# Kernel optimization log

Hardware: AMD Instinct MI355X
Metric: run time of the kernel (lower is better)

Reference implementation:

```python
import jax, jax.numpy as jnp
import numpy as np

D_MODEL = 1024
N_HEAD = 16
STRIDE = 1024
SEQ = STRIDE + 1  # time_mask is (stride+1, stride+1) -> N must equal stride+1
BATCH = 4
EPS = 1e-5


def layer_norm(x, g, b):
    mu = jnp.mean(x, axis=-1, keepdims=True)
    var = jnp.var(x, axis=-1, keepdims=True)
    return (x - mu) * jax.lax.rsqrt(var + EPS) * g + b


def quick_gelu(x):
    return x * jax.nn.sigmoid(1.702 * x)


def setup_inputs() -> dict:
    key = jax.random.key(0)
    ks = jax.random.split(key, 12)
    C = D_MODEL
    s = 0.02
    return {
        "x": jax.random.normal(ks[0], (SEQ, BATCH, C), dtype=jnp.float32),
        "qkv_w": jax.random.normal(ks[1], (3 * C, C), dtype=jnp.float32) * s,
        "proj_w": jax.random.normal(ks[2], (C, C), dtype=jnp.float32) * s,
        "proj_b": jnp.zeros((C,), dtype=jnp.float32),
        "ln1_g": jnp.ones((C,), dtype=jnp.float32),
        "ln1_b": jnp.zeros((C,), dtype=jnp.float32),
        "ln2_g": jnp.ones((C,), dtype=jnp.float32),
        "ln2_b": jnp.zeros((C,), dtype=jnp.float32),
        "fc_w": jax.random.normal(ks[3], (4 * C, C), dtype=jnp.float32) * s,
        "fc_b": jnp.zeros((4 * C,), dtype=jnp.float32),
        "cproj_w": jax.random.normal(ks[4], (C, 4 * C), dtype=jnp.float32) * s,
        "cproj_b": jnp.zeros((C,), dtype=jnp.float32),
    }


def _attention(xs, qkv_w, proj_w, proj_b):
    # xs: [N, B, C] (seq-first) -> internal [B, N, C]
    xb = jnp.transpose(xs, (1, 0, 2))
    B, N, C = xb.shape
    H, Dh = N_HEAD, C // N_HEAD
    scale = Dh ** -0.5
    qkv = xb @ qkv_w.T  # [B, N, 3C], no bias (qkv_bias=False)
    qkv = qkv.reshape(B, N, 3, H, Dh).transpose(2, 0, 3, 1, 4)  # [3, B, H, N, Dh]
    q, k, v = qkv[0], qkv[1], qkv[2]
    attn = jnp.einsum("bhnd,bhmd->bhnm", q, k) * scale
    mask = jnp.tril(jnp.ones((N, N), dtype=bool))  # time_mask: causal tril
    attn = jnp.where(mask, attn, -jnp.inf)
    attn = jax.nn.softmax(attn, axis=-1)
    out = jnp.einsum("bhnm,bhmd->bhnd", attn, v)  # [B, H, N, Dh]
    out = out.transpose(0, 2, 1, 3).reshape(B, N, C)
    out = out @ proj_w.T + proj_b
    return jnp.transpose(out, (1, 0, 2)), attn  # back to [N, B, C]


def reference(x, qkv_w, proj_w, proj_b, ln1_g, ln1_b, ln2_g, ln2_b,
              fc_w, fc_b, cproj_w, cproj_b):
    y, attn = _attention(layer_norm(x, ln1_g, ln1_b), qkv_w, proj_w, proj_b)
    x = x + y
    h = layer_norm(x, ln2_g, ln2_b)
    h = quick_gelu(h @ fc_w.T + fc_b) @ cproj_w.T + cproj_b
    x = x + h
    return (x, attn)
```

## Files before the change

### kernel.cpp

```cpp
#include <hip/hip_runtime.h>


typedef unsigned short ushort_t;
typedef __bf16 bf16x8 __attribute__((ext_vector_type(8)));
typedef float f32x4 __attribute__((ext_vector_type(4)));

#define SEQ_N   1025
#define CMODEL  1024
#define NHEAD   16
#define DH      64
#define TTOK    4100
#define MP      4224
#define NPAD    1152
#define BH      64

__device__ __forceinline__ ushort_t f2bf(float f) {
  union { float f; unsigned u; } v; v.f = f;
  unsigned r = v.u + 0x7fffu + ((v.u >> 16) & 1u);
  return (ushort_t)(r >> 16);
}

__device__ __forceinline__ void gl_lds16(const void* g, void* s) {
  __builtin_amdgcn_global_load_lds(
      (const __attribute__((address_space(1))) unsigned int*)g,
      (__attribute__((address_space(3))) unsigned int*)s, 16, 0, 0);
}

__global__ __launch_bounds__(256)
void cvt4(const float* __restrict__ s0, ushort_t* __restrict__ d0,
          const float* __restrict__ s1, ushort_t* __restrict__ d1,
          const float* __restrict__ s2, ushort_t* __restrict__ d2,
          const float* __restrict__ s3, ushort_t* __restrict__ d3) {
  const int b = blockIdx.x;
  const float* s; ushort_t* d; int off;
  if (b < 3072)      { s = s0; d = d0; off = b; }
  else if (b < 4096) { s = s1; d = d1; off = b - 3072; }
  else if (b < 8192) { s = s2; d = d2; off = b - 4096; }
  else               { s = s3; d = d3; off = b - 8192; }
  const int i = (off * 256 + threadIdx.x) * 4;
  const float4 f = *(const float4*)(s + i);
  ushort4 o;
  o.x = f2bf(f.x); o.y = f2bf(f.y); o.z = f2bf(f.z); o.w = f2bf(f.w);
  *(ushort4*)(d + i) = o;
}

__global__ __launch_bounds__(256)
void ln_bf(const float* __restrict__ xin, const float* __restrict__ g,
           const float* __restrict__ bb, ushort_t* __restrict__ out,
           const float* __restrict__ rbias, float* __restrict__ resout) {
  const int t = blockIdx.x;
  const float* row = xin + (size_t)t * CMODEL;
  const int base = threadIdx.x * 4;
  const float4 v = *(const float4*)(row + base);
  float s = v.x + v.y + v.z + v.w;
  float q = v.x * v.x + v.y * v.y + v.z * v.z + v.w * v.w;
#pragma unroll
  for (int off = 32; off > 0; off >>= 1) {
    s += __shfl_down(s, off);
    q += __shfl_down(q, off);
  }
  __shared__ float sh[8];
  const int wave = threadIdx.x >> 6, lane = threadIdx.x & 63;
  if (lane == 0) { sh[wave] = s; sh[4 + wave] = q; }
  __syncthreads();
  if (threadIdx.x == 0) {
    const float ts = sh[0] + sh[1] + sh[2] + sh[3];
    const float tq = sh[4] + sh[5] + sh[6] + sh[7];
    const float mean = ts * (1.f / CMODEL);
    const float var = tq * (1.f / CMODEL) - mean * mean;
    sh[0] = mean; sh[1] = rsqrtf(var + 1e-5f);
  }
  __syncthreads();
  const float mean = sh[0], rstd = sh[1];
  const float4 gg = *(const float4*)(g + base);
  const float4 bv = *(const float4*)(bb + base);
  ushort4 o;
  o.x = f2bf((v.x - mean) * rstd * gg.x + bv.x);
  o.y = f2bf((v.y - mean) * rstd * gg.y + bv.y);
  o.z = f2bf((v.z - mean) * rstd * gg.z + bv.z);
  o.w = f2bf((v.w - mean) * rstd * gg.w + bv.w);
  *(ushort4*)(out + (size_t)t * CMODEL + base) = o;
  if (resout) {
    const float4 rb = *(const float4*)(rbias + base);
    float4 ro;
    ro.x = v.x + rb.x; ro.y = v.y + rb.y; ro.z = v.z + rb.z; ro.w = v.w + rb.w;
    *(float4*)(resout + (size_t)t * CMODEL + base) = ro;
  }
}

template <int EPI>
__global__ __launch_bounds__(256)
void gemm_bt(const ushort_t* __restrict__ A, int lda,
             const ushort_t* __restrict__ B, int ldb,
             int K,
             const float* __restrict__ bias, const float* __restrict__ res,
             float* __restrict__ outf, ushort_t* __restrict__ outb,
             ushort_t* __restrict__ oq, ushort_t* __restrict__ ok,
             ushort_t* __restrict__ ovt) {
  __shared__ __align__(16) ushort_t lsA[128 * 32];
  __shared__ __align__(16) ushort_t lsB[128 * 32];
  const int tid = threadIdx.x;
  const int wave = tid >> 6, lane = tid & 63;
  const int lr = lane & 15, quad = lane >> 4;

  const int gx = gridDim.x, gy = gridDim.y;
  const int nwg = gx * gy * gridDim.z;
  int lin = blockIdx.x + gx * (blockIdx.y + gy * blockIdx.z);
  lin = (lin & 7) * (nwg >> 3) + (lin >> 3);
  const int bx = lin % gx;
  const int byz = lin / gx;
  const int by = byz % gy;
  const int bz = byz / gy;

  const int tM = by * 128, tN = bx * 128;
  const int kbase = bz * K;
  const int waveM = (wave >> 1) * 64, waveN = (wave & 1) * 64;

  f32x4 acc[4][4];
  const f32x4 z4 = {0.f, 0.f, 0.f, 0.f};
#pragma unroll
  for (int i = 0; i < 4; ++i)
#pragma unroll
    for (int j = 0; j < 4; ++j) acc[i][j] = z4;

  for (int k0 = 0; k0 < K; k0 += 32) {
    __syncthreads();
#pragma unroll
    for (int p = 0; p < 2; ++p) {
      const int idx = p * 256 + wave * 64 + lane;
      const int row = idx >> 2, part = idx & 3;
      const int cb = (p * 256 + wave * 64) * 8;
      gl_lds16(A + (size_t)(tM + row) * lda + kbase + k0 + part * 8, lsA + cb);
      gl_lds16(B + (size_t)(tN + row) * ldb + kbase + k0 + part * 8, lsB + cb);
    }
    __syncthreads();
    bf16x8 af[4], bfr[4];
#pragma unroll
    for (int mi = 0; mi < 4; ++mi)
      af[mi] = *(const bf16x8*)(lsA + (waveM + mi * 16 + lr) * 32 + quad * 8);
#pragma unroll
    for (int ni = 0; ni < 4; ++ni)
      bfr[ni] = *(const bf16x8*)(lsB + (waveN + ni * 16 + lr) * 32 + quad * 8);
#pragma unroll
    for (int mi = 0; mi < 4; ++mi)
#pragma unroll
      for (int ni = 0; ni < 4; ++ni)
        acc[mi][ni] = __builtin_amdgcn_mfma_f32_16x16x32_bf16(af[mi], bfr[ni], acc[mi][ni], 0, 0, 0);
  }

#pragma unroll
  for (int mi = 0; mi < 4; ++mi) {
#pragma unroll
    for (int ni = 0; ni < 4; ++ni) {
#pragma unroll
      for (int r = 0; r < 4; ++r) {
        const int m = tM + waveM + mi * 16 + quad * 4 + r;
        const int n = tN + waveN + ni * 16 + lr;
        const float v = acc[mi][ni][r];
        if constexpr (EPI == 0) {
          if (m < TTOK) {
            const int b_ = m & 3, ns = m >> 2;
            const int which = n >> 10, rem = n & 1023, h = rem >> 6, d = rem & 63;
            const int bh = b_ * NHEAD + h;
            const ushort_t bv = f2bf(v);
            if (which == 0)      oq[((size_t)bh * NPAD + ns) * DH + d] = bv;
            else if (which == 1) ok[((size_t)bh * NPAD + ns) * DH + d] = bv;
            else                 ovt[((size_t)bh * DH + d) * NPAD + ns] = bv;
          }
        } else if constexpr (EPI == 3) {
          if (m < TTOK)
            outf[(size_t)m * CMODEL + n] = v + bias[n] + res[(size_t)m * CMODEL + n];
        } else if constexpr (EPI == 4) {
          if (m < TTOK) {
            const float zv = v + bias[n];
            outb[(size_t)m * 4096 + n] = f2bf(zv / (1.f + __expf(-1.702f * zv)));
          }
        } else if constexpr (EPI == 5) {
          if (m < TTOK)
            atomicAdd(outf + (size_t)m * CMODEL + n, v);
        }
      }
    }
  }
}

__global__ __launch_bounds__(256)
void attn_fused(const ushort_t* __restrict__ qb, const ushort_t* __restrict__ kb,
                const ushort_t* __restrict__ vtb, float* __restrict__ attn,
                ushort_t* __restrict__ ao) {
  __shared__ __align__(16) char smem[34816 + 17408 + 512];
  ushort_t* lsK  = (ushort_t*)smem;
  ushort_t* lsP  = (ushort_t*)smem;
  float*    lpart = (float*)smem;
  ushort_t* lsQV = (ushort_t*)(smem + 34816);
  float*    linvs = (float*)(smem + 34816 + 17408);

  int lin = blockIdx.x + 64 * blockIdx.y;
  lin = (lin & 7) * 72 + (lin >> 3);
  const int bh = lin / 9;
  const int iT = 8 - (lin % 9);
  const int tM = iT * 128;
  const int tid = threadIdx.x;
  const int wave = tid >> 6, lane = tid & 63;
  const int lr = lane & 15, quad = lane >> 4;
  const int waveM = (wave >> 1) * 64, waveN = (wave & 1) * 64;

  const ushort_t* Qg = qb + (size_t)bh * NPAD * DH;
  const ushort_t* Kg = kb + (size_t)bh * NPAD * DH;
  const ushort_t* Vg = vtb + (size_t)bh * DH * NPAD;
  float* attn_h = attn + (size_t)bh * ((size_t)SEQ_N * SEQ_N);

#pragma unroll
  for (int p = 0; p < 4; ++p) {
    const int c = p * 256 + wave * 64 + lane;
    const int ks = c >> 9, n = (c >> 2) & 127, part = c & 3;
    gl_lds16(Qg + (size_t)(tM + n) * DH + ks * 32 + part * 8,
             lsQV + (size_t)(p * 256 + wave * 64) * 8);
  }
  __syncthreads();
  bf16x8 aq[4][2];
#pragma unroll
  for (int mi = 0; mi < 4; ++mi)
#pragma unroll
    for (int ks = 0; ks < 2; ++ks)
      aq[mi][ks] = *(const bf16x8*)(lsQV + ks * 4096 + (waveM + mi * 16 + lr) * 32 + quad * 8);
  __syncthreads();

  f32x4 acc[4][4];
  const f32x4 z4 = {0.f, 0.f, 0.f, 0.f};

  float lsum[4][4];
#pragma unroll
  for (int mi = 0; mi < 4; ++mi)
#pragma unroll
    for (int r = 0; r < 4; ++r) lsum[mi][r] = 0.f;

  for (int j = 0; j <= iT; ++j) {
    __syncthreads();
#pragma unroll
    for (int p = 0; p < 4; ++p) {
      const int c = p * 256 + wave * 64 + lane;
      const int ks = c >> 9, n = (c >> 2) & 127, part = c & 3;
      gl_lds16(Kg + (size_t)(j * 128 + n) * DH + ks * 32 + part * 8,
               lsK + (size_t)(p * 256 + wave * 64) * 8);
    }
    __syncthreads();
#pragma unroll
    for (int mi = 0; mi < 4; ++mi)
#pragma unroll
      for (int ni = 0; ni < 4; ++ni) acc[mi][ni] = z4;
    __builtin_amdgcn_s_setprio(1);
#pragma unroll
    for (int ks = 0; ks < 2; ++ks) {
      bf16x8 bk[4];
#pragma unroll
      for (int ni = 0; ni < 4; ++ni)
        bk[ni] = *(const bf16x8*)(lsK + ks * 4096 + (waveN + ni * 16 + lr) * 32 + quad * 8);
#pragma unroll
      for (int mi = 0; mi < 4; ++mi)
#pragma unroll
        for (int ni = 0; ni < 4; ++ni)
          acc[mi][ni] = __builtin_amdgcn_mfma_f32_16x16x32_bf16(aq[mi][ks], bk[ni], acc[mi][ni], 0, 0, 0);
    }
    __builtin_amdgcn_s_setprio(0);
#pragma unroll
    for (int mi = 0; mi < 4; ++mi)
#pragma unroll
      for (int ni = 0; ni < 4; ++ni)
#pragma unroll
        for (int r = 0; r < 4; ++r) {
          const int row = tM + waveM + mi * 16 + quad * 4 + r;
          const int col = j * 128 + waveN + ni * 16 + lr;
          if (col <= row) lsum[mi][r] += __expf(acc[mi][ni][r] * 0.125f);
        }
  }
#pragma unroll
  for (int mi = 0; mi < 4; ++mi)
#pragma unroll
    for (int r = 0; r < 4; ++r) {
      float s = lsum[mi][r];
      s += __shfl_xor(s, 1); s += __shfl_xor(s, 2);
      s += __shfl_xor(s, 4); s += __shfl_xor(s, 8);
      lsum[mi][r] = s;
    }
  __syncthreads();
  if (lr == 0) {
    const int wx = wave & 1;
#pragma unroll
    for (int mi = 0; mi < 4; ++mi)
#pragma unroll
      for (int r = 0; r < 4; ++r)
        lpart[wx * 128 + waveM + mi * 16 + quad * 4 + r] = lsum[mi][r];
  }
  __syncthreads();
  if (tid < 128) linvs[tid] = 1.0f / (lpart[tid] + lpart[128 + tid]);
  __syncthreads();
  float linv[4][4];
#pragma unroll
  for (int mi = 0; mi < 4; ++mi)
#pragma unroll
    for (int r = 0; r < 4; ++r)
      linv[mi][r] = linvs[waveM + mi * 16 + quad * 4 + r];

  f32x4 oacc[2][4];
#pragma unroll
  for (int i = 0; i < 2; ++i)
#pragma unroll
    for (int j = 0; j < 4; ++j) oacc[i][j] = z4;
  const int prow = wave * 32;
  const int wrow = wave * 32;
  const int lcol = lane;

  for (int j = 0; j <= iT; ++j) {
    __syncthreads();
#pragma unroll
    for (int p = 0; p < 4; ++p) {
      const int c = p * 256 + wave * 64 + lane;
      const int ks = c >> 9, n = (c >> 2) & 127, part = c & 3;
      gl_lds16(Kg + (size_t)(j * 128 + n) * DH + ks * 32 + part * 8,
               lsK + (size_t)(p * 256 + wave * 64) * 8);
    }
#pragma unroll
    for (int p = 0; p < 4; ++p) {
      const int c = p * 256 + tid;
      const int n = c >> 4, klc = c & 15;
      const uint4 v = *(const uint4*)(Vg + (size_t)n * NPAD + j * 128 + klc * 8);
      *(uint4*)(lsQV + (size_t)n * 136 + klc * 8) = v;
    }
    __syncthreads();
#pragma unroll
    for (int mi = 0; mi < 4; ++mi)
#pragma unroll
      for (int ni = 0; ni < 4; ++ni) acc[mi][ni] = z4;
    __builtin_amdgcn_s_setprio(1);
#pragma unroll
    for (int ks = 0; ks < 2; ++ks) {
      bf16x8 bk[4];
#pragma unroll
      for (int ni = 0; ni < 4; ++ni)
        bk[ni] = *(const bf16x8*)(lsK + ks * 4096 + (waveN + ni * 16 + lr) * 32 + quad * 8);
#pragma unroll
      for (int mi = 0; mi < 4; ++mi)
#pragma unroll
        for (int ni = 0; ni < 4; ++ni)
          acc[mi][ni] = __builtin_amdgcn_mfma_f32_16x16x32_bf16(aq[mi][ks], bk[ni], acc[mi][ni], 0, 0, 0);
    }
    __builtin_amdgcn_s_setprio(0);
    __syncthreads();
#pragma unroll
    for (int mi = 0; mi < 4; ++mi)
#pragma unroll
      for (int ni = 0; ni < 4; ++ni)
#pragma unroll
        for (int r = 0; r < 4; ++r) {
          const int rowl = waveM + mi * 16 + quad * 4 + r;
          const int coll = waveN + ni * 16 + lr;
          const int row = tM + rowl;
          const int col = j * 128 + coll;
          const float pv = (col <= row) ? __expf(acc[mi][ni][r] * 0.125f) * linv[mi][r] : 0.f;
          lsP[(size_t)rowl * 136 + coll] = f2bf(pv);
        }
    __syncthreads();
    __builtin_amdgcn_s_setprio(1);
#pragma unroll
    for (int ks = 0; ks < 4; ++ks) {
      bf16x8 ap[2], bv[4];
#pragma unroll
      for (int mi2 = 0; mi2 < 2; ++mi2)
        ap[mi2] = *(const bf16x8*)(lsP + (size_t)(prow + mi2 * 16 + lr) * 136 + ks * 32 + quad * 8);
#pragma unroll
      for (int ni = 0; ni < 4; ++ni)
        bv[ni] = *(const bf16x8*)(lsQV + (size_t)(ni * 16 + lr) * 136 + ks * 32 + quad * 8);
#pragma unroll
      for (int mi2 = 0; mi2 < 2; ++mi2)
#pragma unroll
        for (int ni = 0; ni < 4; ++ni)
          oacc[mi2][ni] = __builtin_amdgcn_mfma_f32_16x16x32_bf16(ap[mi2], bv[ni], oacc[mi2][ni], 0, 0, 0);
    }
    __builtin_amdgcn_s_setprio(0);
#pragma unroll 8
    for (int rr = 0; rr < 32; ++rr) {
      const int grow = tM + wrow + rr;
      if (grow >= SEQ_N) break;
      const ushort_t* lrow = lsP + (size_t)(wrow + rr) * 136;
#pragma unroll
      for (int cb = 0; cb < 2; ++cb) {
        const int gcol = j * 128 + cb * 64 + lcol;
        union { unsigned u; float f; } cv;
        cv.u = ((unsigned)lrow[cb * 64 + lcol]) << 16;
        if (gcol < SEQ_N)
          __builtin_nontemporal_store(cv.f, attn_h + (size_t)grow * SEQ_N + gcol);
      }
    }
  }

  const int b_ = bh >> 4, h = bh & 15;
#pragma unroll
  for (int mi2 = 0; mi2 < 2; ++mi2)
#pragma unroll
    for (int ni = 0; ni < 4; ++ni)
#pragma unroll
      for (int r = 0; r < 4; ++r) {
        const int row = tM + prow + mi2 * 16 + quad * 4 + r;
        const int d = ni * 16 + lr;
        if (row < SEQ_N)
          ao[((size_t)row * 4 + b_) * CMODEL + h * DH + d] = f2bf(oacc[mi2][ni][r]);
      }

  const int c0 = tM + 128;
  if (c0 <= 1024) {
    const int width = 1025 - c0;
    for (int r = wave; r < 128; r += 4) {
      float* rp = attn_h + (size_t)(tM + r) * SEQ_N + c0;
      int pre = ((16 - (int)(((uintptr_t)rp) & 15)) >> 2) & 3;
      if (pre > width) pre = width;
      for (int c = lane; c < pre; c += 64) rp[c] = 0.f;
      const int body = (width - pre) >> 2;
      f32x4* bp = (f32x4*)(rp + pre);
      const f32x4 zf4 = {0.f, 0.f, 0.f, 0.f};
      for (int c = lane; c < body; c += 64) __builtin_nontemporal_store(zf4, bp + c);
      for (int c = pre + body * 4 + lane; c < width; c += 64) rp[c] = 0.f;
    }
  }
}

extern "C" void kernel_launch(void* const* d_in, const int* in_sizes, int n_in,
                              void* d_out, int out_size, void* d_ws, size_t ws_size,
                              hipStream_t stream) {
  const float* x       = (const float*)d_in[0];
  const float* qkv_w   = (const float*)d_in[1];
  const float* proj_w  = (const float*)d_in[2];
  const float* proj_b  = (const float*)d_in[3];
  const float* ln1_g   = (const float*)d_in[4];
  const float* ln1_b   = (const float*)d_in[5];
  const float* ln2_g   = (const float*)d_in[6];
  const float* ln2_b   = (const float*)d_in[7];
  const float* fc_w    = (const float*)d_in[8];
  const float* fc_b    = (const float*)d_in[9];
  const float* cproj_w = (const float*)d_in[10];
  const float* cproj_b = (const float*)d_in[11];

  float* out_x = (float*)d_out;
  float* out_attn = out_x + (size_t)TTOK * CMODEL;

  char* p = (char*)d_ws;
  auto alloc = [&](size_t bytes) { char* r = p; p += (bytes + 255) & ~(size_t)255; return r; };
  ushort_t* ln1x  = (ushort_t*)alloc((size_t)MP * CMODEL * 2);
  ushort_t* wqkv  = (ushort_t*)alloc((size_t)3072 * 1024 * 2);
  ushort_t* wproj = (ushort_t*)alloc((size_t)1024 * 1024 * 2);
  ushort_t* wfc   = (ushort_t*)alloc((size_t)4096 * 1024 * 2);
  ushort_t* wcpr  = (ushort_t*)alloc((size_t)1024 * 4096 * 2);
  ushort_t* qb    = (ushort_t*)alloc((size_t)BH * NPAD * DH * 2);
  ushort_t* kb    = (ushort_t*)alloc((size_t)BH * NPAD * DH * 2);
  ushort_t* vtb   = (ushort_t*)alloc((size_t)BH * DH * NPAD * 2);
  ushort_t* aob   = (ushort_t*)alloc((size_t)MP * CMODEL * 2);
  float*    x1    = (float*)alloc((size_t)MP * CMODEL * 4);
  ushort_t* ln2x  = (ushort_t*)alloc((size_t)MP * CMODEL * 2);
  ushort_t* hb    = (ushort_t*)alloc((size_t)MP * 4096 * 2);
  (void)ws_size; (void)in_sizes; (void)n_in; (void)out_size;

  cvt4<<<12288, 256, 0, stream>>>(qkv_w, wqkv, proj_w, wproj, fc_w, wfc, cproj_w, wcpr);

  ln_bf<<<TTOK, 256, 0, stream>>>(x, ln1_g, ln1_b, ln1x, proj_b, x1);

  gemm_bt<0><<<dim3(24, 33, 1), 256, 0, stream>>>(ln1x, 1024, wqkv, 1024, 1024,
      nullptr, nullptr, nullptr, nullptr, qb, kb, vtb);

  attn_fused<<<dim3(64, 9), 256, 0, stream>>>(qb, kb, vtb, out_attn, aob);

  gemm_bt<5><<<dim3(8, 33, 2), 256, 0, stream>>>(aob, 1024, wproj, 1024, 512,
      nullptr, nullptr, x1, nullptr, nullptr, nullptr, nullptr);

  ln_bf<<<TTOK, 256, 0, stream>>>(x1, ln2_g, ln2_b, ln2x, cproj_b, out_x);

  gemm_bt<4><<<dim3(32, 33, 1), 256, 0, stream>>>(ln2x, 1024, wfc, 1024, 1024,
      fc_b, nullptr, nullptr, hb, nullptr, nullptr, nullptr);

  gemm_bt<5><<<dim3(8, 33, 2), 256, 0, stream>>>(hb, 4096, wcpr, 4096, 2048,
      nullptr, nullptr, out_x, nullptr, nullptr, nullptr, nullptr);
}
```

Before: 743.0 us.

## Add 256x256-tile 8-wave GEMM with staged LDS pipeline for QKV and FC

Adds a new GEMM kernel that uses 256x256 output tiles, 512 threads, and a double-buffered, XOR-swizzled LDS layout filled by direct global-to-LDS loads. Its K loop is split into phases separated by barriers and raised wave priority, so that loads are interleaved with MFMA work. The kernel replaces the 128-tile GEMM for the QKV projection and the FC+GELU layers, with the aim of more reuse per tile and better MFMA utilization. The larger M tiles need the LN output buffers padded to 4352 rows. Fewer workgroups (204 and 272) may leave parts of the GPU idle, and the rows read from the new padding are uninitialized.

```diff
diff --git a/kernel.cpp b/kernel.cpp
--- a/kernel.cpp
+++ b/kernel.cpp
@@ -11,6 +11,7 @@
 #define DH      64
 #define TTOK    4100
 #define MP      4224
+#define MP256   4352
 #define NPAD    1152
 #define BH      64
 
@@ -25,6 +26,10 @@
       (const __attribute__((address_space(1))) unsigned int*)g,
       (__attribute__((address_space(3))) unsigned int*)s, 16, 0, 0);
 }
+
+#define PHB() do { __builtin_amdgcn_sched_barrier(0); \
+                   __builtin_amdgcn_s_barrier();      \
+                   __builtin_amdgcn_sched_barrier(0); } while (0)
 
 __global__ __launch_bounds__(256)
 void cvt4(const float* __restrict__ s0, ushort_t* __restrict__ d0,
@@ -89,6 +94,171 @@
 }
 
 template <int EPI>
+__global__ __launch_bounds__(512, 2)
+void gemm256(const ushort_t* __restrict__ A, int lda,
+             const ushort_t* __restrict__ B, int ldb, int K,
+             const float* __restrict__ bias, ushort_t* __restrict__ outb,
+             ushort_t* __restrict__ oq, ushort_t* __restrict__ ok,
+             ushort_t* __restrict__ ovt) {
+  __shared__ __align__(16) ushort_t lds[4][256 * 64];
+  const int tid = threadIdx.x;
+  const int wave = tid >> 6, lane = tid & 63;
+  const int lr = lane & 15, quad = lane >> 4;
+  const int wm = wave >> 2, wn = wave & 3;
+  const int tM = blockIdx.y * 256, tN = blockIdx.x * 256;
+  const int NT = K >> 6;
+
+  const ushort_t* pA[4]; const ushort_t* pB[4]; int ldsOff[4];
+#pragma unroll
+  for (int li = 0; li < 4; ++li) {
+    const int slot = li * 512 + tid;
+    const int row = slot >> 3, sl = slot & 7;
+    pA[li] = A + (size_t)(tM + row) * lda + ((sl ^ (row & 7)) << 3);
+    pB[li] = B + (size_t)(tN + row) * ldb + ((sl ^ (row & 7)) << 3);
+    ldsOff[li] = (li * 512 + wave * 64) * 8;
+  }
+
+  f32x4 acc[8][4];
+  const f32x4 z4 = {0.f, 0.f, 0.f, 0.f};
+#pragma unroll
+  for (int i = 0; i < 8; ++i)
+#pragma unroll
+    for (int j = 0; j < 4; ++j) acc[i][j] = z4;
+
+  const int arow = wm * 128 + lr;
+  const int brow = wn * 64 + lr;
+  const int swz  = (lr & 7) << 3;
+  const int cq   = quad * 8;
+
+#pragma unroll
+  for (int li = 0; li < 4; ++li) gl_lds16(pA[li], &lds[0][ldsOff[li]]);
+#pragma unroll
+  for (int li = 0; li < 4; ++li) gl_lds16(pB[li], &lds[1][ldsOff[li]]);
+#pragma unroll
+  for (int li = 0; li < 4; ++li) gl_lds16(pA[li] + 64, &lds[2][ldsOff[li]]);
+#pragma unroll
+  for (int li = 0; li < 4; ++li) gl_lds16(pB[li] + 64, &lds[3][ldsOff[li]]);
+  asm volatile("s_waitcnt vmcnt(8)" ::: "memory");
+  PHB();
+
+  for (int t = 0; t < NT; ++t) {
+    const int cur = t & 1;
+    const ushort_t* As = lds[cur * 2 + 0];
+    const ushort_t* Bs = lds[cur * 2 + 1];
+    bf16x8 a[4][2], b[4][2];
+
+#pragma unroll
+    for (int mi = 0; mi < 4; ++mi)
+#pragma unroll
+      for (int ks = 0; ks < 2; ++ks)
+        a[mi][ks] = *(const bf16x8*)(As + (arow + mi * 16) * 64 + ((ks * 32 + cq) ^ swz));
+#pragma unroll
+    for (int ni = 0; ni < 2; ++ni)
+#pragma unroll
+      for (int ks = 0; ks < 2; ++ks)
+        b[ni][ks] = *(const bf16x8*)(Bs + (brow + ni * 16) * 64 + ((ks * 32 + cq) ^ swz));
+    PHB();
+    __builtin_amdgcn_s_setprio(1);
+#pragma unroll
+    for (int mi = 0; mi < 4; ++mi)
+#pragma unroll
+      for (int ni = 0; ni < 2; ++ni)
+#pragma unroll
+        for (int ks = 0; ks < 2; ++ks)
+          acc[mi][ni] = __builtin_amdgcn_mfma_f32_16x16x32_bf16(a[mi][ks], b[ni][ks], acc[mi][ni], 0, 0, 0);
+    __builtin_amdgcn_s_setprio(0);
+    PHB();
+
+#pragma unroll
+    for (int ni = 2; ni < 4; ++ni)
+#pragma unroll
+      for (int ks = 0; ks < 2; ++ks)
+        b[ni][ks] = *(const bf16x8*)(Bs + (brow + ni * 16) * 64 + ((ks * 32 + cq) ^ swz));
+    PHB();
+    __builtin_amdgcn_s_setprio(1);
+#pragma unroll
+    for (int mi = 0; mi < 4; ++mi)
+#pragma unroll
+      for (int ni = 2; ni < 4; ++ni)
+#pragma unroll
+        for (int ks = 0; ks < 2; ++ks)
+          acc[mi][ni] = __builtin_amdgcn_mfma_f32_16x16x32_bf16(a[mi][ks], b[ni][ks], acc[mi][ni], 0, 0, 0);
+    __builtin_amdgcn_s_setprio(0);
+    PHB();
+
+#pragma unroll
+    for (int mi = 0; mi < 4; ++mi)
+#pragma unroll
+      for (int ks = 0; ks < 2; ++ks)
+        a[mi][ks] = *(const bf16x8*)(As + (arow + (mi + 4) * 16) * 64 + ((ks * 32 + cq) ^ swz));
+    PHB();
+    __builtin_amdgcn_s_setprio(1);
+#pragma unroll
+    for (int mi = 0; mi < 4; ++mi)
+#pragma unroll
+      for (int ni = 0; ni < 2; ++ni)
+#pragma unroll
+        for (int ks = 0; ks < 2; ++ks)
+          acc[mi + 4][ni] = __builtin_amdgcn_mfma_f32_16x16x32_bf16(a[mi][ks], b[ni][ks], acc[mi + 4][ni], 0, 0, 0);
+    __builtin_amdgcn_s_setprio(0);
+    PHB();
+
+    if (t + 2 < NT) {
+      const int ko = (t + 2) * 64;
+#pragma unroll
+      for (int li = 0; li < 4; ++li) gl_lds16(pA[li] + ko, &lds[cur * 2 + 0][ldsOff[li]]);
+#pragma unroll
+      for (int li = 0; li < 4; ++li) gl_lds16(pB[li] + ko, &lds[cur * 2 + 1][ldsOff[li]]);
+    }
+    PHB();
+    __builtin_amdgcn_s_setprio(1);
+#pragma unroll
+    for (int mi = 0; mi < 4; ++mi)
+#pragma unroll
+      for (int ni = 2; ni < 4; ++ni)
+#pragma unroll
+        for (int ks = 0; ks < 2; ++ks)
+          acc[mi + 4][ni] = __builtin_amdgcn_mfma_f32_16x16x32_bf16(a[mi][ks], b[ni][ks], acc[mi + 4][ni], 0, 0, 0);
+    __builtin_amdgcn_s_setprio(0);
+    if (t + 2 < NT) {
+      asm volatile("s_waitcnt vmcnt(8)" ::: "memory");
+    } else {
+      asm volatile("s_waitcnt vmcnt(0)" ::: "memory");
+    }
+    PHB();
+  }
+
+#pragma unroll
+  for (int mi = 0; mi < 8; ++mi) {
+#pragma unroll
+    for (int ni = 0; ni < 4; ++ni) {
+#pragma unroll
+      for (int r = 0; r < 4; ++r) {
+        const int m = tM + wm * 128 + mi * 16 + quad * 4 + r;
+        const int n = tN + wn * 64 + ni * 16 + lr;
+        const float v = acc[mi][ni][r];
+        if constexpr (EPI == 0) {
+          if (m < TTOK) {
+            const int b_ = m & 3, ns = m >> 2;
+            const int which = n >> 10, rem = n & 1023, h = rem >> 6, d = rem & 63;
+            const int bh = b_ * NHEAD + h;
+            const ushort_t bv = f2bf(v);
+            if (which == 0)      oq[((size_t)bh * NPAD + ns) * DH + d] = bv;
+            else if (which == 1) ok[((size_t)bh * NPAD + ns) * DH + d] = bv;
+            else                 ovt[((size_t)bh * DH + d) * NPAD + ns] = bv;
+          }
+        } else if constexpr (EPI == 4) {
+          if (m < TTOK) {
+            const float zv = v + bias[n];
+            outb[(size_t)m * 4096 + n] = f2bf(zv / (1.f + __expf(-1.702f * zv)));
+          }
+        }
+      }
+    }
+  }
+}
+
+template <int EPI>
 __global__ __launch_bounds__(256)
 void gemm_bt(const ushort_t* __restrict__ A, int lda,
              const ushort_t* __restrict__ B, int ldb,
@@ -157,31 +327,14 @@
         const int m = tM + waveM + mi * 16 + quad * 4 + r;
         const int n = tN + waveN + ni * 16 + lr;
         const float v = acc[mi][ni][r];
-        if constexpr (EPI == 0) {
-          if (m < TTOK) {
-            const int b_ = m & 3, ns = m >> 2;
-            const int which = n >> 10, rem = n & 1023, h = rem >> 6, d = rem & 63;
-            const int bh = b_ * NHEAD + h;
-            const ushort_t bv = f2bf(v);
-            if (which == 0)      oq[((size_t)bh * NPAD + ns) * DH + d] = bv;
-            else if (which == 1) ok[((size_t)bh * NPAD + ns) * DH + d] = bv;
-            else                 ovt[((size_t)bh * DH + d) * NPAD + ns] = bv;
-          }
-        } else if constexpr (EPI == 3) {
-          if (m < TTOK)
-            outf[(size_t)m * CMODEL + n] = v + bias[n] + res[(size_t)m * CMODEL + n];
-        } else if constexpr (EPI == 4) {
-          if (m < TTOK) {
-            const float zv = v + bias[n];
-            outb[(size_t)m * 4096 + n] = f2bf(zv / (1.f + __expf(-1.702f * zv)));
-          }
-        } else if constexpr (EPI == 5) {
+        if constexpr (EPI == 5) {
           if (m < TTOK)
             atomicAdd(outf + (size_t)m * CMODEL + n, v);
         }
       }
     }
   }
+  (void)bias; (void)res; (void)outb; (void)oq; (void)ok; (void)ovt;
 }
 
 __global__ __launch_bounds__(256)
@@ -445,7 +598,7 @@
 
   char* p = (char*)d_ws;
   auto alloc = [&](size_t bytes) { char* r = p; p += (bytes + 255) & ~(size_t)255; return r; };
-  ushort_t* ln1x  = (ushort_t*)alloc((size_t)MP * CMODEL * 2);
+  ushort_t* ln1x  = (ushort_t*)alloc((size_t)MP256 * CMODEL * 2);
   ushort_t* wqkv  = (ushort_t*)alloc((size_t)3072 * 1024 * 2);
   ushort_t* wproj = (ushort_t*)alloc((size_t)1024 * 1024 * 2);
   ushort_t* wfc   = (ushort_t*)alloc((size_t)4096 * 1024 * 2);
@@ -455,7 +608,7 @@
   ushort_t* vtb   = (ushort_t*)alloc((size_t)BH * DH * NPAD * 2);
   ushort_t* aob   = (ushort_t*)alloc((size_t)MP * CMODEL * 2);
   float*    x1    = (float*)alloc((size_t)MP * CMODEL * 4);
-  ushort_t* ln2x  = (ushort_t*)alloc((size_t)MP * CMODEL * 2);
+  ushort_t* ln2x  = (ushort_t*)alloc((size_t)MP256 * CMODEL * 2);
   ushort_t* hb    = (ushort_t*)alloc((size_t)MP * 4096 * 2);
   (void)ws_size; (void)in_sizes; (void)n_in; (void)out_size;
 
@@ -463,8 +616,8 @@
 
   ln_bf<<<TTOK, 256, 0, stream>>>(x, ln1_g, ln1_b, ln1x, proj_b, x1);
 
-  gemm_bt<0><<<dim3(24, 33, 1), 256, 0, stream>>>(ln1x, 1024, wqkv, 1024, 1024,
-      nullptr, nullptr, nullptr, nullptr, qb, kb, vtb);
+  gemm256<0><<<dim3(12, 17), 512, 0, stream>>>(ln1x, 1024, wqkv, 1024, 1024,
+      nullptr, nullptr, qb, kb, vtb);
 
   attn_fused<<<dim3(64, 9), 256, 0, stream>>>(qb, kb, vtb, out_attn, aob);
 
@@ -473,8 +626,8 @@
 
   ln_bf<<<TTOK, 256, 0, stream>>>(x1, ln2_g, ln2_b, ln2x, cproj_b, out_x);
 
-  gemm_bt<4><<<dim3(32, 33, 1), 256, 0, stream>>>(ln2x, 1024, wfc, 1024, 1024,
-      fc_b, nullptr, nullptr, hb, nullptr, nullptr, nullptr);
+  gemm256<4><<<dim3(16, 17), 512, 0, stream>>>(ln2x, 1024, wfc, 1024, 1024,
+      fc_b, hb, nullptr, nullptr, nullptr);
 
   gemm_bt<5><<<dim3(8, 33, 2), 256, 0, stream>>>(hb, 4096, wcpr, 4096, 2048,
       nullptr, nullptr, out_x, nullptr, nullptr, nullptr, nullptr);
```

Result: no change. 756.7 us (+1.8%).
